# Kernel tuning notes

Measured on AMD Instinct MI355X. Metric: run time of the kernel, lower is better.

Reference implementation:

```python
import jax, jax.numpy as jnp
import numpy as np

B, MAXN, F, H, T, L = 32, 1024, 215, 256, 8, 3
N = B * MAXN            # 32768 global nodes
E = 524288              # total edges, global indices


def setup_inputs() -> dict:
    key = jax.random.key(0)
    ks = jax.random.split(key, 12)
    s = 0.05
    return {
        "node_features": jax.random.normal(ks[0], (B, MAXN, F), dtype=jnp.float32),
        "edge_index": jax.random.randint(ks[1], (2, E), 0, N, dtype=jnp.int32),
        "edge_type": jax.random.randint(ks[2], (E,), 0, T, dtype=jnp.int32),
        # input projection
        "Wp": jax.random.normal(ks[3], (H, F), dtype=jnp.float32) * s,
        "bp": jax.random.normal(ks[4], (H,), dtype=jnp.float32) * s,
        # per-layer, per-edge-type message linears
        "Wm": jax.random.normal(ks[5], (L, T, H, H), dtype=jnp.float32) * s,
        "bm": jax.random.normal(ks[6], (L, T, H), dtype=jnp.float32) * s,
        # per-layer GRUCell params (torch layout: [r|z|n] stacked, 3H rows)
        "Wih": jax.random.normal(ks[7], (L, 3 * H, H), dtype=jnp.float32) * s,
        "Whh": jax.random.normal(ks[8], (L, 3 * H, H), dtype=jnp.float32) * s,
        "bih": jax.random.normal(ks[9], (L, 3 * H), dtype=jnp.float32) * s,
        "bhh": jax.random.normal(ks[10], (L, 3 * H), dtype=jnp.float32) * s,
    }


def _gru_cell(x, h, Wih, Whh, bih, bhh):
    # torch.nn.GRUCell math
    gi = x @ Wih.T + bih            # (N, 3H)
    gh = h @ Whh.T + bhh            # (N, 3H)
    i_r, i_z, i_n = jnp.split(gi, 3, axis=-1)
    h_r, h_z, h_n = jnp.split(gh, 3, axis=-1)
    r = jax.nn.sigmoid(i_r + h_r)
    z = jax.nn.sigmoid(i_z + h_z)
    n = jnp.tanh(i_n + r * h_n)
    return (1.0 - z) * n + z * h


def reference(node_features, edge_index, edge_type, Wp, bp, Wm, bm, Wih, Whh, bih, bhh):
    # flatten batch of graphs into global node array, project to hidden
    h = node_features.reshape(-1, F) @ Wp.T + bp          # (N, H)
    src, dst = edge_index[0], edge_index[1]
    for l in range(L):
        # apply all T type-specific linears to every node once (equivalent to
        # the per-edge-type mask+gather+Linear loop), then gather per edge
        Ht = jnp.einsum('nd,ted->nte', h, Wm[l]) + bm[l]  # (N, T, H)
        msg = Ht[src, edge_type]                           # (E, H) gather
        m = jax.ops.segment_sum(msg, dst, num_segments=N)  # scatter-add (N, H)
        h = _gru_cell(m, h, Wih[l], Whh[l], bih[l], bhh[l])
        # dropout is identity in eval mode
    # readout: full graphs -> sum each graph's node block
    return h.reshape(B, MAXN, H).sum(axis=1)               # (B, H)
```

## Files before the change

kernel.cpp:

```cpp
#include <hip/hip_runtime.h>

#define N_NODES 32768
#define E_EDGES 524288
#define F_IN    215
#define H_DIM   256
#define T_TYPES 8
#define L_LAYERS 3
#define B_GRAPHS 32
#define MAXN_   1024
#define NT_BINS (N_NODES * T_TYPES)

typedef float  f32x4  __attribute__((ext_vector_type(4)));
typedef __bf16 bf16x8 __attribute__((ext_vector_type(8)));

__device__ __forceinline__ unsigned short f2bf(float f) {
  union { float f; unsigned u; } v; v.f = f;
  unsigned r = v.u + 0x7fffu + ((v.u >> 16) & 1u);
  return (unsigned short)(r >> 16);
}
__device__ __forceinline__ float bf2f(unsigned short h) {
  union { unsigned u; float f; } v; v.u = ((unsigned)h) << 16;
  return v.f;
}
__device__ __forceinline__ float bflo(unsigned u) { union { unsigned x; float f; } v; v.x = u << 16; return v.f; }
__device__ __forceinline__ float bfhi(unsigned u) { union { unsigned x; float f; } v; v.x = u & 0xffff0000u; return v.f; }

typedef const __attribute__((address_space(1))) unsigned int* gas_ptr;
typedef __attribute__((address_space(3))) unsigned int* las_ptr;
__device__ __forceinline__ void gload_lds16(const unsigned short* g, unsigned short* l) {
  __builtin_amdgcn_global_load_lds((gas_ptr)g, (las_ptr)l, 16, 0, 0);
}

__device__ __forceinline__ void acc16(float* a, const uint4 v, const uint4 w) {
  a[0]  += bflo(v.x); a[1]  += bfhi(v.x);
  a[2]  += bflo(v.y); a[3]  += bfhi(v.y);
  a[4]  += bflo(v.z); a[5]  += bfhi(v.z);
  a[6]  += bflo(v.w); a[7]  += bfhi(v.w);
  a[8]  += bflo(w.x); a[9]  += bfhi(w.x);
  a[10] += bflo(w.y); a[11] += bfhi(w.y);
  a[12] += bflo(w.z); a[13] += bfhi(w.z);
  a[14] += bflo(w.w); a[15] += bfhi(w.w);
}

static constexpr size_t OFF_BIG     = 0;
static constexpr size_t REL_CURSOR  = 1048576;
static constexpr size_t REL_BSUM    = 2097152;
static constexpr size_t REL_WPPAD   = 33554432;
static constexpr size_t REL_HALT    = 50331648;
static constexpr size_t REL_OFFS    = 100663296;
static constexpr size_t REL_SORTED  = 104857600;
static constexpr size_t OFF_H_B     = 134217728;
static constexpr size_t OFF_M_B     = 150994944;
static constexpr size_t OFF_WMB     = 167772160;
static constexpr size_t OFF_WIH     = 170917888;
static constexpr size_t OFF_WHH     = 172097536;
static constexpr size_t WS_REQUIRED = 173277184;

__global__ void hist_kernel(const int* __restrict__ dst, const int* __restrict__ et,
                            int* __restrict__ cnt) {
  int e = blockIdx.x * 256 + threadIdx.x;
  atomicAdd(&cnt[dst[e] * T_TYPES + et[e]], 1);
}

__global__ __launch_bounds__(1024) void scan1(const int* __restrict__ cnt,
                                              int* __restrict__ offs,
                                              int* __restrict__ bsum) {
  __shared__ int wsum[16];
  const int t = threadIdx.x, lane = t & 63, wid = t >> 6;
  const int idx = blockIdx.x * 1024 + t;
  const int v = cnt[idx];
  int x = v;
  #pragma unroll
  for (int off = 1; off < 64; off <<= 1) {
    int u = __shfl_up(x, off, 64);
    if (lane >= off) x += u;
  }
  if (lane == 63) wsum[wid] = x;
  __syncthreads();
  int wbase = 0;
  for (int i = 0; i < wid; ++i) wbase += wsum[i];
  offs[idx] = wbase + x - v;
  if (t == 1023) bsum[blockIdx.x] = wbase + x;
}

__global__ __launch_bounds__(256) void scan2(int* __restrict__ bsum) {
  __shared__ int wsum[4];
  const int t = threadIdx.x, lane = t & 63, wid = t >> 6;
  const int v = bsum[t];
  int x = v;
  #pragma unroll
  for (int off = 1; off < 64; off <<= 1) {
    int u = __shfl_up(x, off, 64);
    if (lane >= off) x += u;
  }
  if (lane == 63) wsum[wid] = x;
  __syncthreads();
  int wbase = 0;
  for (int i = 0; i < wid; ++i) wbase += wsum[i];
  __syncthreads();
  bsum[t] = wbase + x - v;
}

__global__ __launch_bounds__(1024) void scan3(int* __restrict__ offs,
                                              const int* __restrict__ bsum,
                                              int* __restrict__ cursor) {
  const int idx = blockIdx.x * 1024 + threadIdx.x;
  const int o = offs[idx] + bsum[blockIdx.x];
  offs[idx] = o;
  cursor[idx] = o;
  if (idx == 0) offs[NT_BINS] = E_EDGES;
}

__global__ void reorder_kernel(const int* __restrict__ src, const int* __restrict__ dst,
                               const int* __restrict__ et, int* __restrict__ cursor,
                               unsigned short* __restrict__ sorted) {
  int e = blockIdx.x * 256 + threadIdx.x;
  int key = dst[e] * T_TYPES + et[e];
  int p = atomicAdd(&cursor[key], 1);
  sorted[p] = (unsigned short)src[e];
}

__global__ void cvt_weights(const float* __restrict__ a, const float* __restrict__ b,
                            const float* __restrict__ c,
                            unsigned short* __restrict__ oa, unsigned short* __restrict__ ob,
                            unsigned short* __restrict__ oc,
                            int na, int nb, int nc) {
  int i = blockIdx.x * 256 + threadIdx.x;
  if (i < na) { oa[i] = f2bf(a[i]); return; }
  int j = i - na;
  if (j < nb) { ob[j] = f2bf(b[j]); return; }
  int k = j - nb;
  if (k < nc) oc[k] = f2bf(c[k]);
}

__global__ void pad_cvt(const float* __restrict__ in, unsigned short* __restrict__ out,
                        int rows, int cin) {
  int i = blockIdx.x * 256 + threadIdx.x;
  if (i >= rows * 256) return;
  int r = i >> 8, c = i & 255;
  out[i] = (c < cin) ? f2bf(in[(size_t)r * cin + c]) : (unsigned short)0;
}

__global__ __launch_bounds__(256, 2) void gemm_bt(
    const unsigned short* __restrict__ A,
    const unsigned short* __restrict__ W,
    const float* __restrict__ bias,
    unsigned short* __restrict__ C,
    int M, int K) {
  __shared__ unsigned short As[128 * 32];
  __shared__ unsigned short Bs[128 * 32];
  const int tid = threadIdx.x;
  const int lane = tid & 63;
  const int wv = tid >> 6;
  const int lrow = lane & 15;
  const int lquad = lane >> 4;
  const int bm0 = blockIdx.x * 128;
  const int bn0 = blockIdx.y * 128;
  const int srow = wv * 16 + (lane >> 2);
  const int scol = (lane & 3) * 8;

  f32x4 acc[2][8] = {};

  for (int kt = 0; kt < K; kt += 32) {
    #pragma unroll
    for (int i = 0; i < 2; ++i) {
      const int row = srow + i * 64;
      gload_lds16(A + (size_t)(bm0 + row) * K + kt + scol, &As[row * 32 + scol]);
      gload_lds16(W + (size_t)(bn0 + row) * K + kt + scol, &Bs[row * 32 + scol]);
    }
    __syncthreads();
    bf16x8 af[2], bfr[8];
    #pragma unroll
    for (int mt = 0; mt < 2; ++mt)
      af[mt] = *(const bf16x8*)(&As[(wv * 32 + mt * 16 + lrow) * 32 + lquad * 8]);
    #pragma unroll
    for (int nt = 0; nt < 8; ++nt)
      bfr[nt] = *(const bf16x8*)(&Bs[(nt * 16 + lrow) * 32 + lquad * 8]);
    #pragma unroll
    for (int mt = 0; mt < 2; ++mt)
      #pragma unroll
      for (int nt = 0; nt < 8; ++nt)
        acc[mt][nt] = __builtin_amdgcn_mfma_f32_16x16x32_bf16(af[mt], bfr[nt], acc[mt][nt], 0, 0, 0);
    __syncthreads();
  }

  #pragma unroll
  for (int mt = 0; mt < 2; ++mt) {
    #pragma unroll
    for (int r = 0; r < 4; ++r) {
      const int grow = bm0 + wv * 32 + mt * 16 + lquad * 4 + r;
      #pragma unroll
      for (int nt = 0; nt < 8; ++nt) {
        const int gcol = bn0 + nt * 16 + lrow;
        float v = acc[mt][nt][r] + (bias ? bias[gcol] : 0.f);
        C[(size_t)grow * M + gcol] = f2bf(v);
      }
    }
  }
}

__global__ __launch_bounds__(512, 4) void msg_gemm(
    const int* __restrict__ offs, const unsigned short* __restrict__ sorted,
    const unsigned short* __restrict__ hb, const unsigned short* __restrict__ Wt_l,
    const float* __restrict__ bm_l, unsigned short* __restrict__ m) {
  constexpr int CH = 2568;
  __shared__ unsigned short Ss[8 * CH];
  __shared__ unsigned short Bs[2][256 * 32];
  __shared__ unsigned short idxS[2048];
  __shared__ int offsS[516];
  const int tid = threadIdx.x;
  const int lane = tid & 63;
  const int wv = tid >> 6;
  const int lrow = lane & 15;
  const int lquad = lane >> 4;
  const int wrow = wv & 3;
  const int wcol = wv >> 2;
  const int bm0 = blockIdx.x * 64;
  const int gg = wv * 4 + lquad;
  const int brow = tid >> 2;
  const int bcol = (tid & 3) * 8;

  const int gseg0 = offs[bm0 * 8];
  const int gseg1 = offs[bm0 * 8 + 512];
  const int seg = gseg1 - gseg0;
  for (int i = tid; i < 513; i += 512) offsS[i] = offs[bm0 * 8 + i];
  const int segc = seg < 2048 ? seg : 2048;
  for (int i = tid; i < segc; i += 512) idxS[i] = sorted[gseg0 + i];
  const bool useLds = (seg <= 2048);
  const unsigned short* ip = useLds ? (const unsigned short*)idxS : (sorted + gseg0);
  __syncthreads();

  f32x4 acc[8] = {};
  int buf = 0;

  for (int t = 0; t < T_TYPES; ++t) {
    #pragma unroll
    for (int step = 0; step < 2; ++step) {
      const int dloc = gg + step * 32;
      const int beg = offsS[dloc * 8 + t] - gseg0;
      const int end = offsS[dloc * 8 + t + 1] - gseg0;
      float a[16];
      #pragma unroll
      for (int j = 0; j < 16; ++j) a[j] = 0.f;
      int e = beg;
      if (e + 2 <= end) {
        int s0 = ip[e], s1 = ip[e + 1];
        const unsigned short* h0 = hb + (size_t)s0 * H_DIM + lrow * 16;
        const unsigned short* h1 = hb + (size_t)s1 * H_DIM + lrow * 16;
        uint4 pv0 = *(const uint4*)h0, pw0 = *(const uint4*)(h0 + 8);
        uint4 pv1 = *(const uint4*)h1, pw1 = *(const uint4*)(h1 + 8);
        e += 2;
        for (; e + 2 <= end; e += 2) {
          const int n0 = ip[e], n1 = ip[e + 1];
          const unsigned short* g0 = hb + (size_t)n0 * H_DIM + lrow * 16;
          const unsigned short* g1 = hb + (size_t)n1 * H_DIM + lrow * 16;
          const uint4 nv0 = *(const uint4*)g0, nw0 = *(const uint4*)(g0 + 8);
          const uint4 nv1 = *(const uint4*)g1, nw1 = *(const uint4*)(g1 + 8);
          acc16(a, pv0, pw0);
          acc16(a, pv1, pw1);
          pv0 = nv0; pw0 = nw0; pv1 = nv1; pw1 = nw1;
        }
        acc16(a, pv0, pw0);
        acc16(a, pv1, pw1);
      }
      if (e < end) {
        const int s0 = ip[e];
        const unsigned short* h0 = hb + (size_t)s0 * H_DIM + lrow * 16;
        acc16(a, *(const uint4*)h0, *(const uint4*)(h0 + 8));
      }
      union { unsigned short us[16]; uint4 q[2]; } ob;
      #pragma unroll
      for (int j = 0; j < 16; ++j) ob.us[j] = f2bf(a[j]);
      uint4* p = (uint4*)&Ss[(lrow >> 1) * CH + dloc * 40 + (lrow & 1) * 16];
      p[0] = ob.q[0];
      p[1] = ob.q[1];
    }
    const unsigned short* Wt = Wt_l + (size_t)t * 65536;
    gload_lds16(Wt + (size_t)brow * 256 + bcol, &Bs[buf][brow * 32 + bcol]);
    gload_lds16(Wt + (size_t)(brow + 128) * 256 + bcol, &Bs[buf][(brow + 128) * 32 + bcol]);
    __syncthreads();
    for (int kc = 0; kc < 8; ++kc) {
      if (kc < 7) {
        gload_lds16(Wt + (size_t)brow * 256 + (kc + 1) * 32 + bcol,
                    &Bs[buf ^ 1][brow * 32 + bcol]);
        gload_lds16(Wt + (size_t)(brow + 128) * 256 + (kc + 1) * 32 + bcol,
                    &Bs[buf ^ 1][(brow + 128) * 32 + bcol]);
      }
      const bf16x8 af = *(const bf16x8*)(&Ss[kc * CH + (wrow * 16 + lrow) * 40 + lquad * 8]);
      #pragma unroll
      for (int nt = 0; nt < 8; ++nt) {
        const bf16x8 b = *(const bf16x8*)(&Bs[buf][((wcol * 8 + nt) * 16 + lrow) * 32 + lquad * 8]);
        acc[nt] = __builtin_amdgcn_mfma_f32_16x16x32_bf16(af, b, acc[nt], 0, 0, 0);
      }
      buf ^= 1;
      __syncthreads();
    }
  }

  float cnt[4][8];
  #pragma unroll
  for (int r = 0; r < 4; ++r) {
    const int dl = wrow * 16 + lquad * 4 + r;
    #pragma unroll
    for (int t = 0; t < 8; ++t)
      cnt[r][t] = (float)(offsS[dl * 8 + t + 1] - offsS[dl * 8 + t]);
  }
  #pragma unroll
  for (int nt = 0; nt < 8; ++nt) {
    const int gcol = wcol * 128 + nt * 16 + lrow;
    float bmv[8];
    #pragma unroll
    for (int t = 0; t < 8; ++t) bmv[t] = bm_l[t * H_DIM + gcol];
    #pragma unroll
    for (int r = 0; r < 4; ++r) {
      const int grow = bm0 + wrow * 16 + lquad * 4 + r;
      float v = acc[nt][r];
      #pragma unroll
      for (int t = 0; t < 8; ++t) v += cnt[r][t] * bmv[t];
      m[(size_t)grow * H_DIM + gcol] = f2bf(v);
    }
  }
}

__global__ __launch_bounds__(256, 3) void gru_fused(
    const unsigned short* __restrict__ mB,
    const unsigned short* __restrict__ hin,
    const unsigned short* __restrict__ wih_l,
    const unsigned short* __restrict__ whh_l,
    const float* __restrict__ bih_l,
    const float* __restrict__ bhh_l,
    unsigned short* __restrict__ hout) {
  __shared__ unsigned short Am[64 * 32];
  __shared__ unsigned short Ah[64 * 32];
  const int tid = threadIdx.x;
  const int lane = tid & 63;
  const int wv = tid >> 6;
  const int lrow = lane & 15;
  const int lquad = lane >> 4;
  const int n0 = blockIdx.x * 64;
  const int c0 = blockIdx.y * 64;
  const int arow = tid >> 2;
  const int scol = (tid & 3) * 8;

  f32x4 acc[6][4] = {};

  for (int kt = 0; kt < 256; kt += 32) {
    __syncthreads();
    gload_lds16(mB  + (size_t)(n0 + arow) * 256 + kt + scol, &Am[arow * 32 + scol]);
    gload_lds16(hin + (size_t)(n0 + arow) * 256 + kt + scol, &Ah[arow * 32 + scol]);
    __syncthreads();
    const int wr = c0 + wv * 16 + lrow;
    bf16x8 bfr[6];
    #pragma unroll
    for (int g = 0; g < 3; ++g) {
      bfr[g]     = *(const bf16x8*)(wih_l + (size_t)(g * 256 + wr) * 256 + kt + lquad * 8);
      bfr[g + 3] = *(const bf16x8*)(whh_l + (size_t)(g * 256 + wr) * 256 + kt + lquad * 8);
    }
    #pragma unroll
    for (int mt = 0; mt < 4; ++mt) {
      const bf16x8 am = *(const bf16x8*)(&Am[(mt * 16 + lrow) * 32 + lquad * 8]);
      const bf16x8 ah = *(const bf16x8*)(&Ah[(mt * 16 + lrow) * 32 + lquad * 8]);
      #pragma unroll
      for (int g = 0; g < 6; ++g)
        acc[g][mt] = __builtin_amdgcn_mfma_f32_16x16x32_bf16(g < 3 ? am : ah, bfr[g], acc[g][mt], 0, 0, 0);
    }
  }

  const int c = c0 + wv * 16 + lrow;
  const float b_ir = bih_l[c], b_iz = bih_l[256 + c], b_in = bih_l[512 + c];
  const float b_hr = bhh_l[c], b_hz = bhh_l[256 + c], b_hn = bhh_l[512 + c];
  #pragma unroll
  for (int mt = 0; mt < 4; ++mt) {
    #pragma unroll
    for (int r = 0; r < 4; ++r) {
      const int node = n0 + mt * 16 + lquad * 4 + r;
      const float i_r = acc[0][mt][r] + b_ir;
      const float i_z = acc[1][mt][r] + b_iz;
      const float i_n = acc[2][mt][r] + b_in;
      const float h_r = acc[3][mt][r] + b_hr;
      const float h_z = acc[4][mt][r] + b_hz;
      const float h_n = acc[5][mt][r] + b_hn;
      const float rr = 1.f / (1.f + __expf(-(i_r + h_r)));
      const float zz = 1.f / (1.f + __expf(-(i_z + h_z)));
      const float nn = tanhf(i_n + rr * h_n);
      const float hp = bf2f(hin[(size_t)node * 256 + c]);
      hout[(size_t)node * 256 + c] = f2bf((1.f - zz) * nn + zz * hp);
    }
  }
}

__global__ __launch_bounds__(256) void readout_partial(const unsigned short* __restrict__ hb,
                                                       float* __restrict__ part) {
  const int b = blockIdx.x >> 3;
  const int ch = blockIdx.x & 7;
  const int c = threadIdx.x;
  const unsigned short* base = hb + ((size_t)b * MAXN_ + ch * 128) * H_DIM + c;
  float s = 0.f;
  #pragma unroll 4
  for (int i = 0; i < 128; ++i) s += bf2f(base[(size_t)i * H_DIM]);
  part[(size_t)blockIdx.x * H_DIM + c] = s;
}

__global__ __launch_bounds__(256) void readout_final(const float* __restrict__ part,
                                                     float* __restrict__ out) {
  const int b = blockIdx.x;
  const int c = threadIdx.x;
  float s = 0.f;
  #pragma unroll
  for (int i = 0; i < 8; ++i) s += part[((size_t)b * 8 + i) * H_DIM + c];
  out[b * H_DIM + c] = s;
}

extern "C" void kernel_launch(void* const* d_in, const int* in_sizes, int n_in,
                              void* d_out, int out_size, void* d_ws, size_t ws_size,
                              hipStream_t stream) {
  if (ws_size < WS_REQUIRED) return;

  const float* X   = (const float*)d_in[0];
  const int*   ei  = (const int*)d_in[1];
  const int*   et  = (const int*)d_in[2];
  const float* Wp  = (const float*)d_in[3];
  const float* bp  = (const float*)d_in[4];
  const float* Wm  = (const float*)d_in[5];
  const float* bm  = (const float*)d_in[6];
  const float* Wih = (const float*)d_in[7];
  const float* Whh = (const float*)d_in[8];
  const float* bih = (const float*)d_in[9];
  const float* bhh = (const float*)d_in[10];
  float* out = (float*)d_out;
  char* ws = (char*)d_ws;

  int*            counts = (int*)(ws + OFF_BIG);
  int*            cursor = (int*)(ws + OFF_BIG + REL_CURSOR);
  int*            bsum   = (int*)(ws + OFF_BIG + REL_BSUM);
  unsigned short* xpad   = (unsigned short*)(ws + OFF_BIG);
  unsigned short* wppad  = (unsigned short*)(ws + OFF_BIG + REL_WPPAD);
  unsigned short* h_alt  = (unsigned short*)(ws + OFF_BIG + REL_HALT);
  float*          part   = (float*)(ws + OFF_BIG);
  int*            offs   = (int*)(ws + OFF_BIG + REL_OFFS);
  unsigned short* sorted = (unsigned short*)(ws + OFF_BIG + REL_SORTED);
  unsigned short* h_b    = (unsigned short*)(ws + OFF_H_B);
  unsigned short* m_b    = (unsigned short*)(ws + OFF_M_B);
  unsigned short* wmb    = (unsigned short*)(ws + OFF_WMB);
  unsigned short* wih_b  = (unsigned short*)(ws + OFF_WIH);
  unsigned short* whh_b  = (unsigned short*)(ws + OFF_WHH);

  const int* src = ei;
  const int* dst = ei + E_EDGES;

  hipMemsetAsync(counts, 0, NT_BINS * sizeof(int), stream);
  hist_kernel<<<E_EDGES / 256, 256, 0, stream>>>(dst, et, counts);
  scan1<<<NT_BINS / 1024, 1024, 0, stream>>>(counts, offs, bsum);
  scan2<<<1, 256, 0, stream>>>(bsum);
  scan3<<<NT_BINS / 1024, 1024, 0, stream>>>(offs, bsum, cursor);
  reorder_kernel<<<E_EDGES / 256, 256, 0, stream>>>(src, dst, et, cursor, sorted);

  pad_cvt<<<(N_NODES * 256) / 256, 256, 0, stream>>>(X, xpad, N_NODES, F_IN);
  pad_cvt<<<(256 * 256) / 256, 256, 0, stream>>>(Wp, wppad, 256, F_IN);
  {
    const int na = L_LAYERS * T_TYPES * H_DIM * H_DIM;
    const int nb = L_LAYERS * 3 * H_DIM * H_DIM;
    const int nc = nb;
    cvt_weights<<<(na + nb + nc + 255) / 256, 256, 0, stream>>>(
        Wm, Wih, Whh, wmb, wih_b, whh_b, na, nb, nc);
  }

  gemm_bt<<<dim3(N_NODES / 128, 2), 256, 0, stream>>>(xpad, wppad, bp, h_b, H_DIM, 256);

  for (int l = 0; l < L_LAYERS; ++l) {
    const unsigned short* wm_l  = wmb + (size_t)l * T_TYPES * H_DIM * H_DIM;
    const unsigned short* wih_l = wih_b + (size_t)l * 3 * H_DIM * H_DIM;
    const unsigned short* whh_l = whh_b + (size_t)l * 3 * H_DIM * H_DIM;
    const float* bm_l  = bm + (size_t)l * T_TYPES * H_DIM;
    const float* bih_l = bih + (size_t)l * 3 * H_DIM;
    const float* bhh_l = bhh + (size_t)l * 3 * H_DIM;

    unsigned short* h_cur = (l & 1) ? h_alt : h_b;
    unsigned short* h_nxt = (l & 1) ? h_b : h_alt;

    msg_gemm<<<N_NODES / 64, 512, 0, stream>>>(offs, sorted, h_cur, wm_l, bm_l, m_b);
    gru_fused<<<dim3(N_NODES / 64, 4), 256, 0, stream>>>(
        m_b, h_cur, wih_l, whh_l, bih_l, bhh_l, h_nxt);
  }

  readout_partial<<<B_GRAPHS * 8, 256, 0, stream>>>(h_alt, part);
  readout_final<<<B_GRAPHS, 256, 0, stream>>>(part, out);

  (void)in_sizes; (void)n_in; (void)out_size;
}
```

Before: 628.0 us.

## Stage full 64x256 m/h tiles in LDS once and widen GRU blocks

The GRU kernel now loads the block's whole 64-row m and h tiles (all 256 K columns, padded stride 264) into LDS up front instead of reloading 32-column slices with two barriers per K step. Blocks grow to 512 threads covering 128 output columns, which halves the number of blocks that re-read the same A rows. The previous-h value for the GRU update is read from LDS rather than global memory. LDS use rises to about 67KB per block, which may limit occupancy, and the K loop no longer overlaps A loads with compute.

```diff
diff --git a/kernel.cpp b/kernel.cpp
--- a/kernel.cpp
+++ b/kernel.cpp
@@ -322,7 +322,7 @@
   }
 }
 
-__global__ __launch_bounds__(256, 3) void gru_fused(
+__global__ __launch_bounds__(512, 4) void gru_fused(
     const unsigned short* __restrict__ mB,
     const unsigned short* __restrict__ hin,
     const unsigned short* __restrict__ wih_l,
@@ -330,26 +330,30 @@
     const float* __restrict__ bih_l,
     const float* __restrict__ bhh_l,
     unsigned short* __restrict__ hout) {
-  __shared__ unsigned short Am[64 * 32];
-  __shared__ unsigned short Ah[64 * 32];
+  constexpr int AST = 264;
+  __shared__ unsigned short Am[64 * AST];
+  __shared__ unsigned short Ah[64 * AST];
   const int tid = threadIdx.x;
   const int lane = tid & 63;
   const int wv = tid >> 6;
   const int lrow = lane & 15;
   const int lquad = lane >> 4;
   const int n0 = blockIdx.x * 64;
-  const int c0 = blockIdx.y * 64;
-  const int arow = tid >> 2;
-  const int scol = (tid & 3) * 8;
+  const int c0 = blockIdx.y * 128 + wv * 16;
+
+  #pragma unroll
+  for (int i = 0; i < 4; ++i) {
+    const int idx = i * 512 + tid;
+    const int row = idx >> 5, cc = (idx & 31) * 8;
+    *(uint4*)&Am[row * AST + cc] = *(const uint4*)(mB  + (size_t)(n0 + row) * 256 + cc);
+    *(uint4*)&Ah[row * AST + cc] = *(const uint4*)(hin + (size_t)(n0 + row) * 256 + cc);
+  }
+  __syncthreads();
 
   f32x4 acc[6][4] = {};
 
   for (int kt = 0; kt < 256; kt += 32) {
-    __syncthreads();
-    gload_lds16(mB  + (size_t)(n0 + arow) * 256 + kt + scol, &Am[arow * 32 + scol]);
-    gload_lds16(hin + (size_t)(n0 + arow) * 256 + kt + scol, &Ah[arow * 32 + scol]);
-    __syncthreads();
-    const int wr = c0 + wv * 16 + lrow;
+    const int wr = c0 + lrow;
     bf16x8 bfr[6];
     #pragma unroll
     for (int g = 0; g < 3; ++g) {
@@ -358,22 +362,22 @@
     }
     #pragma unroll
     for (int mt = 0; mt < 4; ++mt) {
-      const bf16x8 am = *(const bf16x8*)(&Am[(mt * 16 + lrow) * 32 + lquad * 8]);
-      const bf16x8 ah = *(const bf16x8*)(&Ah[(mt * 16 + lrow) * 32 + lquad * 8]);
+      const bf16x8 am = *(const bf16x8*)(&Am[(mt * 16 + lrow) * AST + kt + lquad * 8]);
+      const bf16x8 ah = *(const bf16x8*)(&Ah[(mt * 16 + lrow) * AST + kt + lquad * 8]);
       #pragma unroll
       for (int g = 0; g < 6; ++g)
         acc[g][mt] = __builtin_amdgcn_mfma_f32_16x16x32_bf16(g < 3 ? am : ah, bfr[g], acc[g][mt], 0, 0, 0);
     }
   }
 
-  const int c = c0 + wv * 16 + lrow;
+  const int c = c0 + lrow;
   const float b_ir = bih_l[c], b_iz = bih_l[256 + c], b_in = bih_l[512 + c];
   const float b_hr = bhh_l[c], b_hz = bhh_l[256 + c], b_hn = bhh_l[512 + c];
   #pragma unroll
   for (int mt = 0; mt < 4; ++mt) {
     #pragma unroll
     for (int r = 0; r < 4; ++r) {
-      const int node = n0 + mt * 16 + lquad * 4 + r;
+      const int lr = mt * 16 + lquad * 4 + r;
       const float i_r = acc[0][mt][r] + b_ir;
       const float i_z = acc[1][mt][r] + b_iz;
       const float i_n = acc[2][mt][r] + b_in;
@@ -383,8 +387,8 @@
       const float rr = 1.f / (1.f + __expf(-(i_r + h_r)));
       const float zz = 1.f / (1.f + __expf(-(i_z + h_z)));
       const float nn = tanhf(i_n + rr * h_n);
-      const float hp = bf2f(hin[(size_t)node * 256 + c]);
-      hout[(size_t)node * 256 + c] = f2bf((1.f - zz) * nn + zz * hp);
+      const float hp = bf2f(Ah[lr * AST + c]);
+      hout[(size_t)(n0 + lr) * 256 + c] = f2bf((1.f - zz) * nn + zz * hp);
     }
   }
 }
@@ -479,7 +483,7 @@
     unsigned short* h_nxt = (l & 1) ? h_b : h_alt;
 
     msg_gemm<<<N_NODES / 64, 512, 0, stream>>>(offs, sorted, h_cur, wm_l, bm_l, m_b);
-    gru_fused<<<dim3(N_NODES / 64, 4), 256, 0, stream>>>(
+    gru_fused<<<dim3(N_NODES / 64, 2), 512, 0, stream>>>(
         m_b, h_cur, wih_l, whh_l, bih_l, bhh_l, h_nxt);
   }
 
```

Result: slower. 790.6 us (+25.9%).
